# Performance work log

Measured on AMD Instinct MI355X. Metric: run time of the kernel, lower is better.

## Reference

```python
import jax, jax.numpy as jnp
import numpy as np

B, OBS, H, A, E = 131072, 194, 64, 5, 3  # batch, obs dim, hidden, max_action_dim, n event types


def setup_inputs() -> dict:
    key = jax.random.key(0)
    ks = jax.random.split(key, 16)
    s = lambda k, shape, std=0.1: (jax.random.normal(k, shape, dtype=jnp.float32) * std)
    return {
        "x": jax.random.normal(ks[0], (B, OBS), dtype=jnp.float32),
        "action": jax.random.randint(ks[1], (B,), 0, A),
        "W1": s(ks[2], (OBS, H)), "b1": jnp.zeros((H,), jnp.float32),
        "W2": s(ks[3], (H, H)),   "b2": jnp.zeros((H,), jnp.float32),
        "Wh": s(ks[4], (E, H, A), 0.01), "bh": jnp.zeros((E, A), jnp.float32),
        "Wc1": s(ks[5], (OBS, H)), "bc1": jnp.zeros((H,), jnp.float32),
        "Wc2": s(ks[6], (H, H)),   "bc2": jnp.zeros((H,), jnp.float32),
        "Wc3": s(ks[7], (H, 1)),   "bc3": jnp.zeros((1,), jnp.float32),
    }


def reference(x, action, W1, b1, W2, b2, Wh, bh, Wc1, bc1, Wc2, bc2, Wc3, bc3):
    # shared trunk
    feat = jnp.tanh(jnp.tanh(x @ W1 + b1) @ W2 + b2)          # [B, H]
    # route each sample to one of E heads via argmax of first 3 obs dims
    ev = jnp.argmax(x[:, :E], axis=1)                          # [B] int
    all_logits = jnp.einsum('bh,eha->bea', feat, Wh) + bh      # [B, E, A]
    logits = jnp.take_along_axis(
        all_logits, jnp.broadcast_to(ev[:, None, None], (x.shape[0], 1, A)), axis=1
    )[:, 0]                                                    # [B, A]
    logp_all = jax.nn.log_softmax(logits, axis=-1)             # [B, A]
    logp = jnp.take_along_axis(logp_all, action[:, None], axis=1)[:, 0]  # [B]
    entropy = -jnp.sum(jnp.exp(logp_all) * logp_all, axis=-1)  # [B]
    # critic
    value = jnp.tanh(jnp.tanh(x @ Wc1 + bc1) @ Wc2 + bc2) @ Wc3 + bc3    # [B, 1]
    return action, logp, entropy, value
```

## Files before the change

### kernel.cpp

```cpp
#include <hip/hip_runtime.h>
#include <hip/hip_bf16.h>

constexpr int Bt  = 131072;
constexpr int OBS = 194;
constexpr int Hd  = 64;
constexpr int NT  = 256;
constexpr int MT  = 128;
constexpr int KP  = 200;
constexpr int WS  = 72;
constexpr int HS  = 72;
constexpr int LS  = 18;

typedef short bf8   __attribute__((ext_vector_type(8)));
typedef float f32x4 __attribute__((ext_vector_type(4)));

__device__ __forceinline__ short f2bs(float f) {
    union { __hip_bfloat16 h; short s; } u;
    u.h = __float2bfloat16(f);
    return u.s;
}
__device__ __forceinline__ float bs2f(short s) {
    union { short s; __hip_bfloat16 h; } u;
    u.s = s;
    return __bfloat162float(u.h);
}
__device__ __forceinline__ float fast_tanh(float v) {
    v = fminf(fmaxf(v, -15.f), 15.f);
    float e = __expf(2.f * v);
    return (e - 1.f) * __builtin_amdgcn_rcpf(e + 1.f);
}

__global__ void __launch_bounds__(NT) fused_ac(
    const float* __restrict__ x, const int* __restrict__ act_in,
    const float* __restrict__ W1, const float* __restrict__ b1,
    const float* __restrict__ W2, const float* __restrict__ b2,
    const float* __restrict__ Wh, const float* __restrict__ bh,
    const float* __restrict__ Wc1, const float* __restrict__ bc1,
    const float* __restrict__ Wc2, const float* __restrict__ bc2,
    const float* __restrict__ Wc3, const float* __restrict__ bc3,
    float* __restrict__ out)
{
    __shared__ __align__(16) short Wt1[64 * KP];
    __shared__ __align__(16) short W2t[64 * WS];
    __shared__ __align__(16) short WhB[16 * WS];
    __shared__ __align__(16) short hbuf[4][32 * HS];
    __shared__ short logitb[4][32 * LS];
    __shared__ float resb[3][MT];

    const int t  = threadIdx.x;
    const int w  = t >> 6;
    const int l  = t & 63;
    const int q  = l >> 4;
    const int c  = l & 15;
    const int b0 = blockIdx.x * MT;

    if (t < 64) {
        int base = t * KP + 194;
        #pragma unroll
        for (int i = 0; i < 6; ++i) Wt1[base + i] = 0;
    }

    auto stage = [&](const float* Wa, const float* Wb) {
        #pragma unroll 1
        for (int ch = t; ch < (OBS * Hd) / 4; ch += NT) {
            float4 v = reinterpret_cast<const float4*>(Wa)[ch];
            int f = ch * 4, k = f >> 6, n = f & 63;
            Wt1[(n    ) * KP + k] = f2bs(v.x);
            Wt1[(n + 1) * KP + k] = f2bs(v.y);
            Wt1[(n + 2) * KP + k] = f2bs(v.z);
            Wt1[(n + 3) * KP + k] = f2bs(v.w);
        }
        #pragma unroll 1
        for (int ch = t; ch < (Hd * Hd) / 4; ch += NT) {
            float4 v = reinterpret_cast<const float4*>(Wb)[ch];
            int f = ch * 4, k = f >> 6, n = f & 63;
            W2t[(n    ) * WS + k] = f2bs(v.x);
            W2t[(n + 1) * WS + k] = f2bs(v.y);
            W2t[(n + 2) * WS + k] = f2bs(v.z);
            W2t[(n + 3) * WS + k] = f2bs(v.w);
        }
    };
    stage(W1, W2);
    #pragma unroll 1
    for (int i = t; i < 3 * Hd * 5; i += NT) {
        int e = i / 320, r2 = i - e * 320, k = r2 / 5, a = r2 - k * 5;
        WhB[(e * 5 + a) * WS + k] = f2bs(Wh[i]);
    }
    if (t < 64) WhB[15 * WS + t] = f2bs(Wc3[t]);
    __syncthreads();

    bf8 af[2][7];
    {
        const size_t row0 = (size_t)(b0 + w * 32 + c) * OBS;
        #pragma unroll
        for (int s = 0; s < 2; ++s) {
            const float* xr = x + row0 + (size_t)(s * 16) * OBS;
            #pragma unroll
            for (int kb = 0; kb < 6; ++kb) {
                const float2* p = reinterpret_cast<const float2*>(xr + kb * 32 + q * 8);
                float2 v0 = p[0], v1 = p[1], v2 = p[2], v3 = p[3];
                bf8 a;
                a[0] = f2bs(v0.x); a[1] = f2bs(v0.y); a[2] = f2bs(v1.x); a[3] = f2bs(v1.y);
                a[4] = f2bs(v2.x); a[5] = f2bs(v2.y); a[6] = f2bs(v3.x); a[7] = f2bs(v3.y);
                af[s][kb] = a;
            }
            bf8 a6 = {0, 0, 0, 0, 0, 0, 0, 0};
            if (q == 0) {
                float2 v = *reinterpret_cast<const float2*>(xr + 192);
                a6[0] = f2bs(v.x); a6[1] = f2bs(v.y);
            }
            af[s][6] = a6;
        }
    }

    short* hw = hbuf[w];

    auto trunk = [&](const float* __restrict__ ba, const float* __restrict__ bb) {
        f32x4 acc[2][4];
        #pragma unroll
        for (int s = 0; s < 2; ++s)
            #pragma unroll
            for (int nt = 0; nt < 4; ++nt) acc[s][nt] = f32x4{0.f, 0.f, 0.f, 0.f};
        #pragma unroll
        for (int kb = 0; kb < 7; ++kb) {
            #pragma unroll
            for (int nt = 0; nt < 4; ++nt) {
                bf8 bw;
                if (kb < 6)
                    bw = *reinterpret_cast<const bf8*>(&Wt1[(nt * 16 + c) * KP + kb * 32 + q * 8]);
                else if (q == 0)
                    bw = *reinterpret_cast<const bf8*>(&Wt1[(nt * 16 + c) * KP + 192]);
                else
                    bw = bf8{0, 0, 0, 0, 0, 0, 0, 0};
                acc[0][nt] = __builtin_amdgcn_mfma_f32_16x16x32_bf16(af[0][kb], bw, acc[0][nt], 0, 0, 0);
                acc[1][nt] = __builtin_amdgcn_mfma_f32_16x16x32_bf16(af[1][kb], bw, acc[1][nt], 0, 0, 0);
            }
        }
        #pragma unroll
        for (int nt = 0; nt < 4; ++nt) {
            float bias = ba[nt * 16 + c];
            #pragma unroll
            for (int s = 0; s < 2; ++s)
                #pragma unroll
                for (int r = 0; r < 4; ++r)
                    hw[(s * 16 + q * 4 + r) * HS + nt * 16 + c] = f2bs(fast_tanh(acc[s][nt][r] + bias));
        }
        #pragma unroll
        for (int s = 0; s < 2; ++s)
            #pragma unroll
            for (int nt = 0; nt < 4; ++nt) acc[s][nt] = f32x4{0.f, 0.f, 0.f, 0.f};
        #pragma unroll
        for (int kb = 0; kb < 2; ++kb) {
            bf8 ha[2];
            #pragma unroll
            for (int s = 0; s < 2; ++s)
                ha[s] = *reinterpret_cast<const bf8*>(&hw[(s * 16 + c) * HS + kb * 32 + q * 8]);
            #pragma unroll
            for (int nt = 0; nt < 4; ++nt) {
                bf8 bw = *reinterpret_cast<const bf8*>(&W2t[(nt * 16 + c) * WS + kb * 32 + q * 8]);
                acc[0][nt] = __builtin_amdgcn_mfma_f32_16x16x32_bf16(ha[0], bw, acc[0][nt], 0, 0, 0);
                acc[1][nt] = __builtin_amdgcn_mfma_f32_16x16x32_bf16(ha[1], bw, acc[1][nt], 0, 0, 0);
            }
        }
        #pragma unroll
        for (int nt = 0; nt < 4; ++nt) {
            float bias = bb[nt * 16 + c];
            #pragma unroll
            for (int s = 0; s < 2; ++s)
                #pragma unroll
                for (int r = 0; r < 4; ++r)
                    hw[(s * 16 + q * 4 + r) * HS + nt * 16 + c] = f2bs(fast_tanh(acc[s][nt][r] + bias));
        }
    };

    auto smallmm = [&](f32x4 (&lacc)[2]) {
        lacc[0] = f32x4{0.f, 0.f, 0.f, 0.f};
        lacc[1] = f32x4{0.f, 0.f, 0.f, 0.f};
        #pragma unroll
        for (int kb = 0; kb < 2; ++kb) {
            bf8 bw = *reinterpret_cast<const bf8*>(&WhB[c * WS + kb * 32 + q * 8]);
            #pragma unroll
            for (int s = 0; s < 2; ++s) {
                bf8 fa = *reinterpret_cast<const bf8*>(&hw[(s * 16 + c) * HS + kb * 32 + q * 8]);
                lacc[s] = __builtin_amdgcn_mfma_f32_16x16x32_bf16(fa, bw, lacc[s], 0, 0, 0);
            }
        }
    };

    trunk(b1, b2);
    {
        f32x4 lg2[2];
        smallmm(lg2);
        short* lw = logitb[w];
        #pragma unroll
        for (int s = 0; s < 2; ++s)
            #pragma unroll
            for (int r = 0; r < 4; ++r)
                lw[(s * 16 + q * 4 + r) * LS + c] = f2bs(lg2[s][r]);

        int m  = l & 31;
        int gm = b0 + w * 32 + m;
        const float* xr = x + (size_t)gm * OBS;
        float x0 = xr[0], x1 = xr[1], x2 = xr[2];
        int ev = 0; float best = x0;
        if (x1 > best) { best = x1; ev = 1; }
        if (x2 > best) { ev = 2; }
        float lg[5];
        #pragma unroll
        for (int a = 0; a < 5; ++a)
            lg[a] = bs2f(lw[m * LS + ev * 5 + a]) + bh[ev * 5 + a];
        float mx = lg[0];
        #pragma unroll
        for (int a = 1; a < 5; ++a) mx = fmaxf(mx, lg[a]);
        float se = 0.f;
        #pragma unroll
        for (int a = 0; a < 5; ++a) se += __expf(lg[a] - mx);
        float lse = __logf(se) + mx;
        int act = act_in[gm];
        float lsel = lg[0];
        #pragma unroll
        for (int a = 1; a < 5; ++a) lsel = (act == a) ? lg[a] : lsel;
        float ent = 0.f;
        #pragma unroll
        for (int a = 0; a < 5; ++a) { float lp = lg[a] - lse; ent -= __expf(lp) * lp; }
        if (l < 32) { resb[0][w * 32 + m] = lsel - lse; resb[1][w * 32 + m] = ent; }
    }

    __syncthreads();
    stage(Wc1, Wc2);
    __syncthreads();

    trunk(bc1, bc2);
    {
        f32x4 vacc[2];
        smallmm(vacc);
        if (c == 15) {
            float bc3v = bc3[0];
            #pragma unroll
            for (int s = 0; s < 2; ++s)
                #pragma unroll
                for (int r = 0; r < 4; ++r)
                    resb[2][w * 32 + s * 16 + q * 4 + r] = vacc[s][r] + bc3v;
        }
    }

    __syncthreads();
    if (t < MT) {
        int b = b0 + t;
        out[b]          = (float)act_in[b];
        out[Bt + b]     = resb[0][t];
        out[2 * Bt + b] = resb[1][t];
        out[3 * Bt + b] = resb[2][t];
    }
}

extern "C" void kernel_launch(void* const* d_in, const int* in_sizes, int n_in,
                              void* d_out, int out_size, void* d_ws, size_t ws_size,
                              hipStream_t stream) {
    const float* x   = (const float*)d_in[0];
    const int*   act = (const int*)  d_in[1];
    const float* W1  = (const float*)d_in[2];
    const float* b1  = (const float*)d_in[3];
    const float* W2  = (const float*)d_in[4];
    const float* b2  = (const float*)d_in[5];
    const float* Wh  = (const float*)d_in[6];
    const float* bh  = (const float*)d_in[7];
    const float* Wc1 = (const float*)d_in[8];
    const float* bc1 = (const float*)d_in[9];
    const float* Wc2 = (const float*)d_in[10];
    const float* bc2 = (const float*)d_in[11];
    const float* Wc3 = (const float*)d_in[12];
    const float* bc3 = (const float*)d_in[13];
    float* out = (float*)d_out;

    dim3 grid(Bt / MT), block(NT);
    hipLaunchKernelGGL(fused_ac, grid, block, 0, stream,
                       x, act, W1, b1, W2, b2, Wh, bh,
                       Wc1, bc1, Wc2, bc2, Wc3, bc3, out);
}
```

Measured before the change: 212.0 us.

## Pre-pack weights into MFMA fragment layout in global memory, drop LDS staging

Adds a prep kernel that converts all weight matrices to bf16 once per call and stores them in a workspace, already arranged in the per-lane MFMA B-fragment order. The main kernel then reads weight fragments straight from global memory (served by cache) instead of having every block stage and transpose W1/W2/Wc1/Wc2/Wh into LDS. This removes the per-block staging work and most block-wide barriers, and cuts LDS use so more blocks can be resident (launch bounds now request 4 per SIMD). Outputs are written per wave. The cost is an extra kernel launch and global/L2 loads inside the MFMA loops, which may add latency.

```diff
diff --git a/kernel.cpp b/kernel.cpp
--- a/kernel.cpp
+++ b/kernel.cpp
@@ -6,10 +6,15 @@
 constexpr int Hd  = 64;
 constexpr int NT  = 256;
 constexpr int MT  = 128;
-constexpr int KP  = 200;
-constexpr int WS  = 72;
 constexpr int HS  = 72;
 constexpr int LS  = 18;
+
+constexpr int W1B_OFF  = 0;
+constexpr int WC1B_OFF = 28672;
+constexpr int W2B_OFF  = 57344;
+constexpr int WC2B_OFF = 65536;
+constexpr int WHB_OFF  = 73728;
+constexpr int WS_SHORTS = 74752;
 
 typedef short bf8   __attribute__((ext_vector_type(8)));
 typedef float f32x4 __attribute__((ext_vector_type(4)));
@@ -30,22 +35,56 @@
     return (e - 1.f) * __builtin_amdgcn_rcpf(e + 1.f);
 }
 
-__global__ void __launch_bounds__(NT) fused_ac(
+__global__ void __launch_bounds__(256) prep(
+    const float* __restrict__ W1, const float* __restrict__ W2,
+    const float* __restrict__ Wh, const float* __restrict__ Wc1,
+    const float* __restrict__ Wc2, const float* __restrict__ Wc3,
+    short* __restrict__ ws)
+{
+    const int gid = blockIdx.x * 256 + threadIdx.x;
+    const int gsz = gridDim.x * 256;
+
+    for (int i = gid; i < 28672; i += gsz) {
+        int j = i & 7, l = (i >> 3) & 63, nt = (i >> 9) & 3, kb = i >> 11;
+        int k = kb * 32 + ((l >> 4) << 3) + j;
+        int n = nt * 16 + (l & 15);
+        short v1 = 0, v2 = 0;
+        if (k < OBS) {
+            v1 = f2bs(W1[k * 64 + n]);
+            v2 = f2bs(Wc1[k * 64 + n]);
+        }
+        ws[W1B_OFF + i]  = v1;
+        ws[WC1B_OFF + i] = v2;
+    }
+    for (int i = gid; i < 8192; i += gsz) {
+        int j = i & 7, l = (i >> 3) & 63, nt = (i >> 9) & 3, kb = i >> 11;
+        int k = kb * 32 + ((l >> 4) << 3) + j;
+        int n = nt * 16 + (l & 15);
+        ws[W2B_OFF + i]  = f2bs(W2[k * 64 + n]);
+        ws[WC2B_OFF + i] = f2bs(Wc2[k * 64 + n]);
+    }
+    for (int i = gid; i < 1024; i += gsz) {
+        int j = i & 7, l = (i >> 3) & 63, kb = i >> 9;
+        int k = kb * 32 + ((l >> 4) << 3) + j;
+        int cc = l & 15;
+        float v;
+        if (cc == 15) v = Wc3[k];
+        else { int e = cc / 5, a = cc - 5 * e; v = Wh[(e * 64 + k) * 5 + a]; }
+        ws[WHB_OFF + i] = f2bs(v);
+    }
+}
+
+__global__ void __launch_bounds__(NT, 4) fused_ac(
     const float* __restrict__ x, const int* __restrict__ act_in,
-    const float* __restrict__ W1, const float* __restrict__ b1,
-    const float* __restrict__ W2, const float* __restrict__ b2,
-    const float* __restrict__ Wh, const float* __restrict__ bh,
-    const float* __restrict__ Wc1, const float* __restrict__ bc1,
-    const float* __restrict__ Wc2, const float* __restrict__ bc2,
-    const float* __restrict__ Wc3, const float* __restrict__ bc3,
+    const float* __restrict__ b1, const float* __restrict__ b2,
+    const float* __restrict__ bh, const float* __restrict__ bc1,
+    const float* __restrict__ bc2, const float* __restrict__ bc3,
+    const short* __restrict__ ws,
     float* __restrict__ out)
 {
-    __shared__ __align__(16) short Wt1[64 * KP];
-    __shared__ __align__(16) short W2t[64 * WS];
-    __shared__ __align__(16) short WhB[16 * WS];
     __shared__ __align__(16) short hbuf[4][32 * HS];
     __shared__ short logitb[4][32 * LS];
-    __shared__ float resb[3][MT];
+    __shared__ float valb[4][32];
 
     const int t  = threadIdx.x;
     const int w  = t >> 6;
@@ -54,40 +93,11 @@
     const int c  = l & 15;
     const int b0 = blockIdx.x * MT;
 
-    if (t < 64) {
-        int base = t * KP + 194;
-        #pragma unroll
-        for (int i = 0; i < 6; ++i) Wt1[base + i] = 0;
-    }
-
-    auto stage = [&](const float* Wa, const float* Wb) {
-        #pragma unroll 1
-        for (int ch = t; ch < (OBS * Hd) / 4; ch += NT) {
-            float4 v = reinterpret_cast<const float4*>(Wa)[ch];
-            int f = ch * 4, k = f >> 6, n = f & 63;
-            Wt1[(n    ) * KP + k] = f2bs(v.x);
-            Wt1[(n + 1) * KP + k] = f2bs(v.y);
-            Wt1[(n + 2) * KP + k] = f2bs(v.z);
-            Wt1[(n + 3) * KP + k] = f2bs(v.w);
-        }
-        #pragma unroll 1
-        for (int ch = t; ch < (Hd * Hd) / 4; ch += NT) {
-            float4 v = reinterpret_cast<const float4*>(Wb)[ch];
-            int f = ch * 4, k = f >> 6, n = f & 63;
-            W2t[(n    ) * WS + k] = f2bs(v.x);
-            W2t[(n + 1) * WS + k] = f2bs(v.y);
-            W2t[(n + 2) * WS + k] = f2bs(v.z);
-            W2t[(n + 3) * WS + k] = f2bs(v.w);
-        }
-    };
-    stage(W1, W2);
-    #pragma unroll 1
-    for (int i = t; i < 3 * Hd * 5; i += NT) {
-        int e = i / 320, r2 = i - e * 320, k = r2 / 5, a = r2 - k * 5;
-        WhB[(e * 5 + a) * WS + k] = f2bs(Wh[i]);
-    }
-    if (t < 64) WhB[15 * WS + t] = f2bs(Wc3[t]);
-    __syncthreads();
+    const bf8* __restrict__ fW1  = reinterpret_cast<const bf8*>(ws + W1B_OFF);
+    const bf8* __restrict__ fWc1 = reinterpret_cast<const bf8*>(ws + WC1B_OFF);
+    const bf8* __restrict__ fW2  = reinterpret_cast<const bf8*>(ws + W2B_OFF);
+    const bf8* __restrict__ fWc2 = reinterpret_cast<const bf8*>(ws + WC2B_OFF);
+    const bf8* __restrict__ fWh  = reinterpret_cast<const bf8*>(ws + WHB_OFF);
 
     bf8 af[2][7];
     {
@@ -115,7 +125,8 @@
 
     short* hw = hbuf[w];
 
-    auto trunk = [&](const float* __restrict__ ba, const float* __restrict__ bb) {
+    auto trunk = [&](const bf8* __restrict__ fa1, const bf8* __restrict__ fa2,
+                     const float* __restrict__ ba, const float* __restrict__ bb) {
         f32x4 acc[2][4];
         #pragma unroll
         for (int s = 0; s < 2; ++s)
@@ -125,13 +136,7 @@
         for (int kb = 0; kb < 7; ++kb) {
             #pragma unroll
             for (int nt = 0; nt < 4; ++nt) {
-                bf8 bw;
-                if (kb < 6)
-                    bw = *reinterpret_cast<const bf8*>(&Wt1[(nt * 16 + c) * KP + kb * 32 + q * 8]);
-                else if (q == 0)
-                    bw = *reinterpret_cast<const bf8*>(&Wt1[(nt * 16 + c) * KP + 192]);
-                else
-                    bw = bf8{0, 0, 0, 0, 0, 0, 0, 0};
+                bf8 bw = fa1[(kb * 4 + nt) * 64 + l];
                 acc[0][nt] = __builtin_amdgcn_mfma_f32_16x16x32_bf16(af[0][kb], bw, acc[0][nt], 0, 0, 0);
                 acc[1][nt] = __builtin_amdgcn_mfma_f32_16x16x32_bf16(af[1][kb], bw, acc[1][nt], 0, 0, 0);
             }
@@ -157,7 +162,7 @@
                 ha[s] = *reinterpret_cast<const bf8*>(&hw[(s * 16 + c) * HS + kb * 32 + q * 8]);
             #pragma unroll
             for (int nt = 0; nt < 4; ++nt) {
-                bf8 bw = *reinterpret_cast<const bf8*>(&W2t[(nt * 16 + c) * WS + kb * 32 + q * 8]);
+                bf8 bw = fa2[(kb * 4 + nt) * 64 + l];
                 acc[0][nt] = __builtin_amdgcn_mfma_f32_16x16x32_bf16(ha[0], bw, acc[0][nt], 0, 0, 0);
                 acc[1][nt] = __builtin_amdgcn_mfma_f32_16x16x32_bf16(ha[1], bw, acc[1][nt], 0, 0, 0);
             }
@@ -178,7 +183,7 @@
         lacc[1] = f32x4{0.f, 0.f, 0.f, 0.f};
         #pragma unroll
         for (int kb = 0; kb < 2; ++kb) {
-            bf8 bw = *reinterpret_cast<const bf8*>(&WhB[c * WS + kb * 32 + q * 8]);
+            bf8 bw = fWh[kb * 64 + l];
             #pragma unroll
             for (int s = 0; s < 2; ++s) {
                 bf8 fa = *reinterpret_cast<const bf8*>(&hw[(s * 16 + c) * HS + kb * 32 + q * 8]);
@@ -187,7 +192,8 @@
         }
     };
 
-    trunk(b1, b2);
+    trunk(fW1, fW2, b1, b2);
+    float r_logp, r_ent;
     {
         f32x4 lg2[2];
         smallmm(lg2);
@@ -223,14 +229,11 @@
         float ent = 0.f;
         #pragma unroll
         for (int a = 0; a < 5; ++a) { float lp = lg[a] - lse; ent -= __expf(lp) * lp; }
-        if (l < 32) { resb[0][w * 32 + m] = lsel - lse; resb[1][w * 32 + m] = ent; }
-    }
-
-    __syncthreads();
-    stage(Wc1, Wc2);
-    __syncthreads();
-
-    trunk(bc1, bc2);
+        r_logp = lsel - lse;
+        r_ent  = ent;
+    }
+
+    trunk(fWc1, fWc2, bc1, bc2);
     {
         f32x4 vacc[2];
         smallmm(vacc);
@@ -240,17 +243,16 @@
             for (int s = 0; s < 2; ++s)
                 #pragma unroll
                 for (int r = 0; r < 4; ++r)
-                    resb[2][w * 32 + s * 16 + q * 4 + r] = vacc[s][r] + bc3v;
-        }
-    }
-
-    __syncthreads();
-    if (t < MT) {
-        int b = b0 + t;
-        out[b]          = (float)act_in[b];
-        out[Bt + b]     = resb[0][t];
-        out[2 * Bt + b] = resb[1][t];
-        out[3 * Bt + b] = resb[2][t];
+                    valb[w][s * 16 + q * 4 + r] = vacc[s][r] + bc3v;
+        }
+    }
+
+    if (l < 32) {
+        int gm = b0 + w * 32 + l;
+        out[gm]          = (float)act_in[gm];
+        out[Bt + gm]     = r_logp;
+        out[2 * Bt + gm] = r_ent;
+        out[3 * Bt + gm] = valb[w][l];
     }
 }
 
@@ -272,9 +274,10 @@
     const float* Wc3 = (const float*)d_in[12];
     const float* bc3 = (const float*)d_in[13];
     float* out = (float*)d_out;
-
-    dim3 grid(Bt / MT), block(NT);
-    hipLaunchKernelGGL(fused_ac, grid, block, 0, stream,
-                       x, act, W1, b1, W2, b2, Wh, bh,
-                       Wc1, bc1, Wc2, bc2, Wc3, bc3, out);
-}
+    short* ws  = (short*)d_ws;
+
+    hipLaunchKernelGGL(prep, dim3(64), dim3(256), 0, stream,
+                       W1, W2, Wh, Wc1, Wc2, Wc3, ws);
+    hipLaunchKernelGGL(fused_ac, dim3(Bt / MT), dim3(NT), 0, stream,
+                       x, act, b1, b2, bh, bc1, bc2, bc3, ws, out);
+}
```

Result: faster. 199.9 us (-5.7%).
